# Kernel optimization log

Measured on AMD Instinct MI355X. Metric: run time of the kernel, lower is better.

The kernel has to match this reference:

```python
import jax, jax.numpy as jnp
import numpy as np

NEG_SLOPE = 0.2
BN_EPS = 1e-5


def _gat_conv(x, src, dst, W, a_src, a_dst, bias, heads, concat):
    # x: [N, Fin], W: [Fin, heads*C], a_src/a_dst: [heads, C]
    N = x.shape[0]
    C = W.shape[1] // heads
    h = (x @ W).reshape(N, heads, C)                       # [N, H, C]
    s_src = jnp.einsum('nhc,hc->nh', h, a_src)             # [N, H]
    s_dst = jnp.einsum('nhc,hc->nh', h, a_dst)             # [N, H]
    e = jax.nn.leaky_relu(s_src[src] + s_dst[dst], NEG_SLOPE)  # [E, H]
    # segment softmax over incoming edges of each destination node
    m = jax.ops.segment_max(e, dst, num_segments=N)
    m = jnp.where(jnp.isfinite(m), m, 0.0)
    ex = jnp.exp(e - m[dst])
    denom = jax.ops.segment_sum(ex, dst, num_segments=N)
    alpha = ex / (denom[dst] + 1e-16)                      # [E, H]
    out = jax.ops.segment_sum(alpha[:, :, None] * h[src], dst, num_segments=N)  # [N,H,C]
    if concat:
        out = out.reshape(N, heads * C)
    else:
        out = out.mean(axis=1)
    return out + bias


def setup_inputs() -> dict:
    key = jax.random.key(0)
    ks = jax.random.split(key, 12)
    N, E, Fin, Ch, H, Fout = 50000, 800000, 128, 32, 4, 2
    Fhid = Ch * H  # 128
    x = jax.random.normal(ks[0], (N, Fin), dtype=jnp.float32)
    edge_index = jax.random.randint(ks[1], (2, E), 0, N, dtype=jnp.int64)
    def glorot(k, shape):
        fan = shape[0] + shape[-1]
        return jax.random.normal(k, shape, dtype=jnp.float32) * jnp.sqrt(2.0 / fan)
    return {
        'x': x,
        'edge_index': edge_index,
        'W1': glorot(ks[2], (Fin, Fhid)),
        'att_src1': glorot(ks[3], (H, Ch)),
        'att_dst1': glorot(ks[4], (H, Ch)),
        'b1': jnp.zeros((Fhid,), jnp.float32),
        'gamma': jnp.ones((Fhid,), jnp.float32),
        'beta': jnp.zeros((Fhid,), jnp.float32),
        'W2': glorot(ks[5], (Fhid, Fout)),
        'att_src2': glorot(ks[6], (1, Fout)),
        'att_dst2': glorot(ks[7], (1, Fout)),
        'b2': jnp.zeros((Fout,), jnp.float32),
    }


def reference(x, edge_index, W1, att_src1, att_dst1, b1, gamma, beta,
              W2, att_src2, att_dst2, b2):
    N = x.shape[0]
    # PyG GATConv adds self-loops by default
    loops = jnp.arange(N, dtype=edge_index.dtype)
    src = jnp.concatenate([edge_index[0], loops])
    dst = jnp.concatenate([edge_index[1], loops])
    h = _gat_conv(x, src, dst, W1, att_src1, att_dst1, b1, heads=4, concat=True)
    # BatchNorm1d (batch statistics, train-mode math)
    mu = h.mean(axis=0)
    var = h.var(axis=0)
    h = (h - mu) * jax.lax.rsqrt(var + BN_EPS) * gamma + beta
    h = jax.nn.elu(h)
    # dropout = 0 (eval)
    out = _gat_conv(h, src, dst, W2, att_src2, att_dst2, b2, heads=1, concat=False)
    return out
```

## Files before the change

### kernel.cpp

```cpp
#include <hip/hip_runtime.h>
#include <hip/hip_bf16.h>
#include <hip/hip_fp16.h>
#include <math.h>

#define FH 128
#define NEG_SLOPE 0.2f
#define BN_EPS 1e-5f
#define NBLK_BN 512

__global__ __launch_bounds__(256) void k_gemm1(
    const float* __restrict__ x, const float* __restrict__ W,
    const float* __restrict__ asrc, const float* __restrict__ adst,
    __half* __restrict__ h1h, float* __restrict__ ssrc, float* __restrict__ sdst,
    int N)
{
    __shared__ float xsT[32][260];
    __shared__ float Ws[32][68];
    const int t = threadIdx.x;
    const int row0 = blockIdx.x * 256;
    const int col0 = blockIdx.y * 64;
    const int tc = t & 7, rg = t >> 3;
    const int c0 = tc * 8, r0 = rg * 8;

    float acc[8][8];
    #pragma unroll
    for (int i = 0; i < 8; ++i)
        #pragma unroll
        for (int j = 0; j < 8; ++j) acc[i][j] = 0.f;

    for (int kc = 0; kc < 128; kc += 32) {
        #pragma unroll
        for (int i = 0; i < 8; ++i) {
            int f4 = i * 256 + t;
            int r = f4 >> 3, kq = (f4 & 7) * 4;
            float4 v = make_float4(0.f, 0.f, 0.f, 0.f);
            if (row0 + r < N) v = *(const float4*)(x + (size_t)(row0 + r) * FH + kc + kq);
            xsT[kq][r] = v.x; xsT[kq + 1][r] = v.y;
            xsT[kq + 2][r] = v.z; xsT[kq + 3][r] = v.w;
        }
        #pragma unroll
        for (int i = 0; i < 2; ++i) {
            int f4 = i * 256 + t;
            int k = f4 >> 4, cq = (f4 & 15) * 4;
            *(float4*)&Ws[k][cq] = *(const float4*)(W + (size_t)(kc + k) * FH + col0 + cq);
        }
        __syncthreads();
        #pragma unroll 4
        for (int k = 0; k < 32; ++k) {
            float4 xa0 = *(const float4*)&xsT[k][r0];
            float4 xa1 = *(const float4*)&xsT[k][r0 + 4];
            float4 wv0 = *(const float4*)&Ws[k][c0];
            float4 wv1 = *(const float4*)&Ws[k][c0 + 4];
            float xr[8] = {xa0.x, xa0.y, xa0.z, xa0.w, xa1.x, xa1.y, xa1.z, xa1.w};
            float wc[8] = {wv0.x, wv0.y, wv0.z, wv0.w, wv1.x, wv1.y, wv1.z, wv1.w};
            #pragma unroll
            for (int i = 0; i < 8; ++i)
                #pragma unroll
                for (int j = 0; j < 8; ++j)
                    acc[i][j] = fmaf(xr[i], wc[j], acc[i][j]);
        }
        __syncthreads();
    }

    const int hg = (col0 + c0) >> 5;
    const int cl = (col0 + c0) & 31;
    float4 as0 = *(const float4*)(asrc + hg * 32 + cl);
    float4 as1 = *(const float4*)(asrc + hg * 32 + cl + 4);
    float4 ad0 = *(const float4*)(adst + hg * 32 + cl);
    float4 ad1 = *(const float4*)(adst + hg * 32 + cl + 4);
    float as[8] = {as0.x, as0.y, as0.z, as0.w, as1.x, as1.y, as1.z, as1.w};
    float ad[8] = {ad0.x, ad0.y, ad0.z, ad0.w, ad1.x, ad1.y, ad1.z, ad1.w};
    float sA[8], dA[8];
    #pragma unroll
    for (int i = 0; i < 8; ++i) {
        float s = 0.f, d = 0.f;
        #pragma unroll
        for (int j = 0; j < 8; ++j) {
            s = fmaf(acc[i][j], as[j], s);
            d = fmaf(acc[i][j], ad[j], d);
        }
        sA[i] = s; dA[i] = d;
    }
    #pragma unroll
    for (int i = 0; i < 8; ++i) {
        sA[i] += __shfl_xor(sA[i], 1, 64); sA[i] += __shfl_xor(sA[i], 2, 64);
        dA[i] += __shfl_xor(dA[i], 1, 64); dA[i] += __shfl_xor(dA[i], 2, 64);
    }
    if ((tc & 3) == 0) {
        #pragma unroll
        for (int i = 0; i < 8; ++i) {
            int row = row0 + r0 + i;
            if (row < N) { ssrc[row * 4 + hg] = sA[i]; sdst[row * 4 + hg] = dA[i]; }
        }
    }
    #pragma unroll
    for (int i = 0; i < 8; ++i) {
        int row = row0 + r0 + i;
        if (row < N) {
            __half2 ph[4];
            ph[0] = __floats2half2_rn(acc[i][0], acc[i][1]);
            ph[1] = __floats2half2_rn(acc[i][2], acc[i][3]);
            ph[2] = __floats2half2_rn(acc[i][4], acc[i][5]);
            ph[3] = __floats2half2_rn(acc[i][6], acc[i][7]);
            *(uint4*)(h1h + (size_t)row * FH + col0 + c0) = *(uint4*)ph;
        }
    }
}

__global__ void k_count(const int* __restrict__ ei, int E, int N, int* __restrict__ deg) {
    int i = blockIdx.x * blockDim.x + threadIdx.x;
    if (i >= E + N) return;
    int d = (i < E) ? ei[E + i] : (i - E);
    atomicAdd(&deg[d], 1);
}

__global__ __launch_bounds__(1024) void k_scan1(const int* __restrict__ deg,
                                                int* __restrict__ rowptr,
                                                int* __restrict__ blksum, int N) {
    int t = threadIdx.x;
    int i = blockIdx.x * 1024 + t;
    int v = (i < N) ? deg[i] : 0;
    int lane = t & 63, w = t >> 6;
    int incl = v;
    #pragma unroll
    for (int off = 1; off < 64; off <<= 1) {
        int tmp = __shfl_up(incl, off, 64);
        if (lane >= off) incl += tmp;
    }
    __shared__ int wsum[16];
    if (lane == 63) wsum[w] = incl;
    __syncthreads();
    if (t == 0) {
        int s = 0;
        for (int k = 0; k < 16; ++k) { int x = wsum[k]; wsum[k] = s; s += x; }
    }
    __syncthreads();
    int excl = incl - v + wsum[w];
    if (i < N) rowptr[i] = excl;
    if (t == 1023) blksum[blockIdx.x] = excl + v;
}

__global__ __launch_bounds__(1024) void k_scan2(const int* __restrict__ blksum,
                                                int* __restrict__ blkoff, int nblk) {
    int t = threadIdx.x;
    int v = (t < nblk) ? blksum[t] : 0;
    int lane = t & 63, w = t >> 6;
    int incl = v;
    #pragma unroll
    for (int off = 1; off < 64; off <<= 1) {
        int tmp = __shfl_up(incl, off, 64);
        if (lane >= off) incl += tmp;
    }
    __shared__ int wsum[16];
    if (lane == 63) wsum[w] = incl;
    __syncthreads();
    if (t == 0) {
        int s = 0;
        for (int k = 0; k < 16; ++k) { int x = wsum[k]; wsum[k] = s; s += x; }
    }
    __syncthreads();
    int excl = incl - v + wsum[w];
    if (t < nblk) blkoff[t] = excl;
    if (t == nblk - 1) blkoff[nblk] = excl + v;
}

__global__ void k_scan3(int* __restrict__ rowptr, const int* __restrict__ blkoff, int N) {
    int i = blockIdx.x * blockDim.x + threadIdx.x;
    if (i > N) return;
    if (i == N) rowptr[N] = blkoff[(N + 1023) >> 10];
    else        rowptr[i] += blkoff[i >> 10];
}

__global__ void k_fill(const int* __restrict__ ei, int E, int N,
                       const int* __restrict__ rowptr, int* __restrict__ deg,
                       const float4* __restrict__ ssrc4, const float4* __restrict__ sdst4,
                       int* __restrict__ csr, float4* __restrict__ alpha4) {
    int i = blockIdx.x * blockDim.x + threadIdx.x;
    if (i >= E + N) return;
    int s, d;
    if (i < E) { s = ei[i]; d = ei[E + i]; }
    else       { s = i - E; d = i - E; }
    int pos = atomicSub(&deg[d], 1) - 1;
    int slot = rowptr[d] + pos;
    csr[slot] = s;
    float4 sv = ssrc4[s];
    float4 dv = sdst4[d];
    float ex = sv.x + dv.x; ex = fmaxf(ex, NEG_SLOPE * ex);
    float ey = sv.y + dv.y; ey = fmaxf(ey, NEG_SLOPE * ey);
    float ez = sv.z + dv.z; ez = fmaxf(ez, NEG_SLOPE * ez);
    float ew = sv.w + dv.w; ew = fmaxf(ew, NEG_SLOPE * ew);
    float4 a;
    a.x = __expf(ex); a.y = __expf(ey); a.z = __expf(ez); a.w = __expf(ew);
    alpha4[slot] = a;
}

__global__ __launch_bounds__(256) void k_agg1(
    const int* __restrict__ rowptr, const int* __restrict__ csr,
    const float* __restrict__ alph, const __half* __restrict__ h1h,
    const float* __restrict__ b1, float* __restrict__ out, int N)
{
    int n = (blockIdx.x * blockDim.x + threadIdx.x) >> 6;
    int lane = threadIdx.x & 63;
    if (n >= N) return;
    int start = rowptr[n];
    int dcnt  = rowptr[n + 1] - start;
    int h = lane >> 4;

    float ax = 0.f, ay = 0.f, l = 0.f;
    const __half2* h1v = (const __half2*)h1h;
    #pragma unroll 4
    for (int j = 0; j < dcnt; ++j) {
        int idx = start + j;
        int s = csr[idx];
        float a = alph[idx * 4 + h];
        l += a;
        float2 v = __half22float2(h1v[((size_t)s << 6) + lane]);
        ax = fmaf(a, v.x, ax);
        ay = fmaf(a, v.y, ay);
    }
    float inv = 1.f / (l + 1e-16f);
    float2 b1v = ((const float2*)b1)[lane];
    float2 o;
    o.x = fmaf(ax, inv, b1v.x);
    o.y = fmaf(ay, inv, b1v.y);
    ((float2*)out)[((size_t)n << 6) + lane] = o;
}

__global__ __launch_bounds__(256) void k_bnstat(const float4* __restrict__ hb4,
                                                float* __restrict__ part_s,
                                                float* __restrict__ part_q, int N) {
    __shared__ float rs[8][128];
    __shared__ float rq[8][128];
    int t = threadIdx.x;
    int rg = t >> 5, c4 = t & 31;
    float sx = 0, sy = 0, sz = 0, sw = 0, qx = 0, qy = 0, qz = 0, qw = 0;
    for (int r = blockIdx.x * 8 + rg; r < N; r += gridDim.x * 8) {
        float4 v = hb4[(size_t)r * 32 + c4];
        sx += v.x; sy += v.y; sz += v.z; sw += v.w;
        qx = fmaf(v.x, v.x, qx); qy = fmaf(v.y, v.y, qy);
        qz = fmaf(v.z, v.z, qz); qw = fmaf(v.w, v.w, qw);
    }
    int c = c4 * 4;
    rs[rg][c] = sx; rs[rg][c+1] = sy; rs[rg][c+2] = sz; rs[rg][c+3] = sw;
    rq[rg][c] = qx; rq[rg][c+1] = qy; rq[rg][c+2] = qz; rq[rg][c+3] = qw;
    __syncthreads();
    for (int k = 4; k; k >>= 1) {
        if (rg < k) {
            rs[rg][c]   += rs[rg+k][c];   rs[rg][c+1] += rs[rg+k][c+1];
            rs[rg][c+2] += rs[rg+k][c+2]; rs[rg][c+3] += rs[rg+k][c+3];
            rq[rg][c]   += rq[rg+k][c];   rq[rg][c+1] += rq[rg+k][c+1];
            rq[rg][c+2] += rq[rg+k][c+2]; rq[rg][c+3] += rq[rg+k][c+3];
        }
        __syncthreads();
    }
    if (t < 128) {
        part_s[(size_t)blockIdx.x * 128 + t] = rs[0][t];
        part_q[(size_t)blockIdx.x * 128 + t] = rq[0][t];
    }
}

__global__ __launch_bounds__(1024) void k_bnred(const float* __restrict__ part_s,
                                                const float* __restrict__ part_q,
                                                const float* __restrict__ gamma,
                                                const float* __restrict__ beta,
                                                float* __restrict__ bnscale,
                                                float* __restrict__ bnshift,
                                                float invN) {
    __shared__ float ls[8][128];
    __shared__ float lq[8][128];
    int t = threadIdx.x;
    int c = t & 127, g = t >> 7;
    float s = 0.f, q = 0.f;
    for (int blk = g; blk < NBLK_BN; blk += 8) {
        s += part_s[(size_t)blk * 128 + c];
        q += part_q[(size_t)blk * 128 + c];
    }
    ls[g][c] = s; lq[g][c] = q;
    __syncthreads();
    for (int k = 4; k; k >>= 1) {
        if (g < k) { ls[g][c] += ls[g + k][c]; lq[g][c] += lq[g + k][c]; }
        __syncthreads();
    }
    if (t < 128) {
        float mu  = ls[0][t] * invN;
        float var = lq[0][t] * invN - mu * mu;
        float sc  = rsqrtf(var + BN_EPS) * gamma[t];
        bnscale[t] = sc;
        bnshift[t] = beta[t] - mu * sc;
    }
}

__global__ __launch_bounds__(256) void k_bn2(const float4* __restrict__ hb4,
                                             const float* __restrict__ bnscale,
                                             const float* __restrict__ bnshift,
                                             const float* __restrict__ W2,
                                             const float* __restrict__ as2,
                                             const float* __restrict__ ad2,
                                             float4* __restrict__ node2, int N) {
    int t = threadIdx.x;
    int rl = t >> 5, c4 = t & 31;
    int r = blockIdx.x * 8 + rl;
    if (r >= N) return;
    int c = c4 * 4;
    float4 sc4 = *(const float4*)(bnscale + c);
    float4 sh4 = *(const float4*)(bnshift + c);
    float4 v = hb4[(size_t)r * 32 + c4];
    float t0 = fmaf(v.x, sc4.x, sh4.x);
    float t1 = fmaf(v.y, sc4.y, sh4.y);
    float t2 = fmaf(v.z, sc4.z, sh4.z);
    float t3 = fmaf(v.w, sc4.w, sh4.w);
    t0 = t0 > 0.f ? t0 : expm1f(t0);
    t1 = t1 > 0.f ? t1 : expm1f(t1);
    t2 = t2 > 0.f ? t2 : expm1f(t2);
    t3 = t3 > 0.f ? t3 : expm1f(t3);
    float d0 = t0 * W2[c * 2]       + t1 * W2[(c + 1) * 2]
             + t2 * W2[(c + 2) * 2] + t3 * W2[(c + 3) * 2];
    float d1 = t0 * W2[c * 2 + 1]       + t1 * W2[(c + 1) * 2 + 1]
             + t2 * W2[(c + 2) * 2 + 1] + t3 * W2[(c + 3) * 2 + 1];
    #pragma unroll
    for (int off = 16; off; off >>= 1) {
        d0 += __shfl_xor(d0, off, 64);
        d1 += __shfl_xor(d1, off, 64);
    }
    if (c4 == 0) {
        float4 o;
        o.x = d0; o.y = d1;
        o.z = d0 * as2[0] + d1 * as2[1];
        o.w = d0 * ad2[0] + d1 * ad2[1];
        node2[r] = o;
    }
}

__global__ __launch_bounds__(256) void k_agg2(const int* __restrict__ rowptr,
                                              const int* __restrict__ csr,
                                              const float4* __restrict__ node2,
                                              const float* __restrict__ b2,
                                              float* __restrict__ out, int N) {
    int gid = blockIdx.x * blockDim.x + threadIdx.x;
    int n = gid >> 4;
    int ln = gid & 15;
    if (n >= N) return;
    int start = rowptr[n];
    int dcnt  = rowptr[n + 1] - start;
    float sdv = node2[n].w;
    float m = -3e38f, l = 0.f, a0 = 0.f, a1 = 0.f;
    for (int j = ln; j < dcnt; j += 16) {
        int s = csr[start + j];
        float4 hv = node2[s];
        float e = hv.z + sdv;
        e = fmaxf(e, NEG_SLOPE * e);
        float nm = fmaxf(m, e);
        float sc = __expf(m - nm);
        float p  = __expf(e - nm);
        a0 = a0 * sc + p * hv.x;
        a1 = a1 * sc + p * hv.y;
        l  = l * sc + p;
        m  = nm;
    }
    #pragma unroll
    for (int off = 8; off; off >>= 1) {
        float mo  = __shfl_xor(m, off, 64);
        float lo  = __shfl_xor(l, off, 64);
        float a0o = __shfl_xor(a0, off, 64);
        float a1o = __shfl_xor(a1, off, 64);
        float nm = fmaxf(m, mo);
        float sc = __expf(m - nm), so = __expf(mo - nm);
        l  = l * sc + lo * so;
        a0 = a0 * sc + a0o * so;
        a1 = a1 * sc + a1o * so;
        m  = nm;
    }
    if (ln == 0) {
        float inv = 1.f / (l + 1e-16f);
        float2 o;
        o.x = fmaf(a0, inv, b2[0]);
        o.y = fmaf(a1, inv, b2[1]);
        ((float2*)out)[n] = o;
    }
}

extern "C" void kernel_launch(void* const* d_in, const int* in_sizes, int n_in,
                              void* d_out, int out_size, void* d_ws, size_t ws_size,
                              hipStream_t stream) {
    const int N = in_sizes[0] / FH;
    const int E = in_sizes[1] / 2;
    const int Etot = E + N;
    const int nblk = (N + 1023) >> 10;

    const float* x     = (const float*)d_in[0];
    const int*   ei    = (const int*)d_in[1];
    const float* W1    = (const float*)d_in[2];
    const float* asrc1 = (const float*)d_in[3];
    const float* adst1 = (const float*)d_in[4];
    const float* b1    = (const float*)d_in[5];
    const float* gamma = (const float*)d_in[6];
    const float* beta  = (const float*)d_in[7];
    const float* W2    = (const float*)d_in[8];
    const float* as2   = (const float*)d_in[9];
    const float* ad2   = (const float*)d_in[10];
    const float* b2    = (const float*)d_in[11];
    float* out = (float*)d_out;

    char* ws = (char*)d_ws;
    size_t off = 0;
    auto nxt = [&](size_t bytes) {
        size_t o = off;
        off += (bytes + 255) & ~(size_t)255;
        return o;
    };
    __half* h1h    = (__half*)(ws + nxt((size_t)N * FH * 2));
    float* hb      = (float*)(ws + nxt((size_t)N * FH * 4));
    float* ssrc1   = (float*)(ws + nxt((size_t)N * 4 * 4));
    float* sdst1   = (float*)(ws + nxt((size_t)N * 4 * 4));
    float* node2   = (float*)(ws + nxt((size_t)N * 4 * 4));
    float* alpha   = (float*)(ws + nxt((size_t)Etot * 4 * 4));
    float* part_s  = (float*)(ws + nxt((size_t)NBLK_BN * 128 * 4));
    float* part_q  = (float*)(ws + nxt((size_t)NBLK_BN * 128 * 4));
    float* bnscale = (float*)(ws + nxt(128 * 4));
    float* bnshift = (float*)(ws + nxt(128 * 4));
    size_t zoff0   = off;
    int*   deg     = (int*)(ws + nxt((size_t)N * 4));
    size_t zbytes  = off - zoff0;
    int*   rowptr  = (int*)(ws + nxt((size_t)(N + 1) * 4));
    int*   csr     = (int*)(ws + nxt((size_t)Etot * 4));
    int*   blksum  = (int*)(ws + nxt((size_t)nblk * 4));
    int*   blkoff  = (int*)(ws + nxt((size_t)(nblk + 1) * 4));

    hipMemsetAsync(ws + zoff0, 0, zbytes, stream);

    dim3 g1((N + 255) / 256, 2);
    k_gemm1<<<g1, 256, 0, stream>>>(x, W1, asrc1, adst1, h1h, ssrc1, sdst1, N);
    k_count<<<(Etot + 255) / 256, 256, 0, stream>>>(ei, E, N, deg);
    k_scan1<<<nblk, 1024, 0, stream>>>(deg, rowptr, blksum, N);
    k_scan2<<<1, 1024, 0, stream>>>(blksum, blkoff, nblk);
    k_scan3<<<(N + 256) / 256, 256, 0, stream>>>(rowptr, blkoff, N);
    k_fill<<<(Etot + 255) / 256, 256, 0, stream>>>(ei, E, N, rowptr, deg,
                                                   (const float4*)ssrc1,
                                                   (const float4*)sdst1,
                                                   csr, (float4*)alpha);
    k_agg1<<<(N + 3) / 4, 256, 0, stream>>>(rowptr, csr, alpha, h1h, b1, hb, N);
    k_bnstat<<<NBLK_BN, 256, 0, stream>>>((const float4*)hb, part_s, part_q, N);
    k_bnred<<<1, 1024, 0, stream>>>(part_s, part_q, gamma, beta, bnscale, bnshift,
                                    1.0f / (float)N);
    k_bn2<<<(N + 7) / 8, 256, 0, stream>>>((const float4*)hb, bnscale, bnshift,
                                           W2, as2, ad2, (float4*)node2, N);
    k_agg2<<<(N * 16 + 255) / 256, 256, 0, stream>>>(rowptr, csr, (const float4*)node2,
                                                     b2, out, N);
}
```

Before: 293.2 us.

## Compute edge attention weights inside aggregation instead of materializing alpha array

Moves the leaky-relu and exp of the layer-1 attention scores out of the CSR fill kernel and into the aggregation kernel. Each wavefront loads up to 64 neighbor indices at a time, computes their four per-head weights in parallel, stages them in shared memory, then runs the gather loop over that shared buffer. This drops the 16-byte-per-edge alpha array write and re-read and the scattered source-score gather in k_fill. The cost is a shared-memory staging step per 64-edge chunk, with wavefront-level rather than block-level synchronisation between writing and reading the staged data.

```diff
diff --git a/kernel.cpp b/kernel.cpp
--- a/kernel.cpp
+++ b/kernel.cpp
@@ -173,50 +173,61 @@
 
 __global__ void k_fill(const int* __restrict__ ei, int E, int N,
                        const int* __restrict__ rowptr, int* __restrict__ deg,
-                       const float4* __restrict__ ssrc4, const float4* __restrict__ sdst4,
-                       int* __restrict__ csr, float4* __restrict__ alpha4) {
+                       int* __restrict__ csr) {
     int i = blockIdx.x * blockDim.x + threadIdx.x;
     if (i >= E + N) return;
     int s, d;
     if (i < E) { s = ei[i]; d = ei[E + i]; }
     else       { s = i - E; d = i - E; }
     int pos = atomicSub(&deg[d], 1) - 1;
-    int slot = rowptr[d] + pos;
-    csr[slot] = s;
-    float4 sv = ssrc4[s];
-    float4 dv = sdst4[d];
-    float ex = sv.x + dv.x; ex = fmaxf(ex, NEG_SLOPE * ex);
-    float ey = sv.y + dv.y; ey = fmaxf(ey, NEG_SLOPE * ey);
-    float ez = sv.z + dv.z; ez = fmaxf(ez, NEG_SLOPE * ez);
-    float ew = sv.w + dv.w; ew = fmaxf(ew, NEG_SLOPE * ew);
-    float4 a;
-    a.x = __expf(ex); a.y = __expf(ey); a.z = __expf(ez); a.w = __expf(ew);
-    alpha4[slot] = a;
+    csr[rowptr[d] + pos] = s;
 }
 
 __global__ __launch_bounds__(256) void k_agg1(
     const int* __restrict__ rowptr, const int* __restrict__ csr,
-    const float* __restrict__ alph, const __half* __restrict__ h1h,
-    const float* __restrict__ b1, float* __restrict__ out, int N)
+    const float4* __restrict__ ssrc4, const float4* __restrict__ sdst4,
+    const __half* __restrict__ h1h, const float* __restrict__ b1,
+    float* __restrict__ out, int N)
 {
+    __shared__ __align__(16) float lal[4][256];
+    __shared__ int lsrc[4][64];
+    int wid  = threadIdx.x >> 6;
+    int lane = threadIdx.x & 63;
     int n = (blockIdx.x * blockDim.x + threadIdx.x) >> 6;
-    int lane = threadIdx.x & 63;
     if (n >= N) return;
     int start = rowptr[n];
     int dcnt  = rowptr[n + 1] - start;
     int h = lane >> 4;
 
+    float4 dv = sdst4[n];
     float ax = 0.f, ay = 0.f, l = 0.f;
     const __half2* h1v = (const __half2*)h1h;
-    #pragma unroll 4
-    for (int j = 0; j < dcnt; ++j) {
-        int idx = start + j;
-        int s = csr[idx];
-        float a = alph[idx * 4 + h];
-        l += a;
-        float2 v = __half22float2(h1v[((size_t)s << 6) + lane]);
-        ax = fmaf(a, v.x, ax);
-        ay = fmaf(a, v.y, ay);
+
+    for (int j0 = 0; j0 < dcnt; j0 += 64) {
+        int j = j0 + lane;
+        if (j < dcnt) {
+            int s = csr[start + j];
+            float4 sv = ssrc4[s];
+            float ex = sv.x + dv.x; ex = fmaxf(ex, NEG_SLOPE * ex);
+            float ey = sv.y + dv.y; ey = fmaxf(ey, NEG_SLOPE * ey);
+            float ez = sv.z + dv.z; ez = fmaxf(ez, NEG_SLOPE * ez);
+            float ew = sv.w + dv.w; ew = fmaxf(ew, NEG_SLOPE * ew);
+            float4 a4;
+            a4.x = __expf(ex); a4.y = __expf(ey);
+            a4.z = __expf(ez); a4.w = __expf(ew);
+            *(float4*)&lal[wid][lane * 4] = a4;
+            lsrc[wid][lane] = s;
+        }
+        int jend = dcnt - j0; if (jend > 64) jend = 64;
+        #pragma unroll 4
+        for (int jj = 0; jj < jend; ++jj) {
+            float a = lal[wid][jj * 4 + h];
+            int s = lsrc[wid][jj];
+            l += a;
+            float2 v = __half22float2(h1v[((size_t)s << 6) + lane]);
+            ax = fmaf(a, v.x, ax);
+            ay = fmaf(a, v.y, ay);
+        }
     }
     float inv = 1.f / (l + 1e-16f);
     float2 b1v = ((const float2*)b1)[lane];
@@ -413,7 +424,6 @@
     float* ssrc1   = (float*)(ws + nxt((size_t)N * 4 * 4));
     float* sdst1   = (float*)(ws + nxt((size_t)N * 4 * 4));
     float* node2   = (float*)(ws + nxt((size_t)N * 4 * 4));
-    float* alpha   = (float*)(ws + nxt((size_t)Etot * 4 * 4));
     float* part_s  = (float*)(ws + nxt((size_t)NBLK_BN * 128 * 4));
     float* part_q  = (float*)(ws + nxt((size_t)NBLK_BN * 128 * 4));
     float* bnscale = (float*)(ws + nxt(128 * 4));
@@ -434,11 +444,9 @@
     k_scan1<<<nblk, 1024, 0, stream>>>(deg, rowptr, blksum, N);
     k_scan2<<<1, 1024, 0, stream>>>(blksum, blkoff, nblk);
     k_scan3<<<(N + 256) / 256, 256, 0, stream>>>(rowptr, blkoff, N);
-    k_fill<<<(Etot + 255) / 256, 256, 0, stream>>>(ei, E, N, rowptr, deg,
-                                                   (const float4*)ssrc1,
-                                                   (const float4*)sdst1,
-                                                   csr, (float4*)alpha);
-    k_agg1<<<(N + 3) / 4, 256, 0, stream>>>(rowptr, csr, alpha, h1h, b1, hb, N);
+    k_fill<<<(Etot + 255) / 256, 256, 0, stream>>>(ei, E, N, rowptr, deg, csr);
+    k_agg1<<<(N + 3) / 4, 256, 0, stream>>>(rowptr, csr, (const float4*)ssrc1,
+                                            (const float4*)sdst1, h1h, b1, hb, N);
     k_bnstat<<<NBLK_BN, 256, 0, stream>>>((const float4*)hb, part_s, part_q, N);
     k_bnred<<<1, 1024, 0, stream>>>(part_s, part_q, gamma, beta, bnscale, bnshift,
                                     1.0f / (float)N);
```

Measured after the change: 291.8 us. Within noise of the previous version (-0.5%).
